# Optimization experiments

Hardware: AMD Instinct MI355X
Metric: run time of the kernel (lower is better)

The kernel has to match this reference:

```python
import jax, jax.numpy as jnp
import numpy as np

N = 50000   # nodes
E = 800000  # edges
D = 128     # input node features
H = 128     # hidden channels
G = 250     # graphs in batch
EPS = 1e-5  # BatchNorm eps


def _lin(k, fi, fo):
    s = 1.0 / np.sqrt(fi)
    return jax.random.uniform(k, (fi, fo), jnp.float32, -s, s)


def setup_inputs() -> dict:
    key = jax.random.key(0)
    ks = jax.random.split(key, 16)
    x = jax.random.normal(ks[0], (N, D), jnp.float32)
    edge_index = jax.random.randint(ks[1], (2, E), 0, N)
    batch = jnp.sort(jax.random.randint(ks[2], (N,), 0, G))
    return {
        "x": x, "edge_index": edge_index, "batch": batch,
        "W1": _lin(ks[3], D, H), "b1": jnp.zeros((H,), jnp.float32),
        "g1": jnp.ones((H,), jnp.float32), "be1": jnp.zeros((H,), jnp.float32),
        "W2": _lin(ks[4], H, H), "b2": jnp.zeros((H,), jnp.float32),
        "g2": jnp.ones((H,), jnp.float32), "be2": jnp.zeros((H,), jnp.float32),
        "W3": _lin(ks[5], H, H), "b3": jnp.zeros((H,), jnp.float32),
        "g3": jnp.ones((H,), jnp.float32), "be3": jnp.zeros((H,), jnp.float32),
        "Wm1": _lin(ks[6], H, H), "bm1": _lin(ks[7], H, 1)[:, 0],
        "Wm2": _lin(ks[8], H, 1), "bm2": _lin(ks[9], 1, 1)[:, 0],
    }


def gcn_conv(x, W, b, src, dst, n):
    # PyG GCNConv: h = x W; add self-loops; symmetric deg^{-1/2} normalization;
    # scatter-add messages from src to dst; add bias.
    h = x @ W                                     # [N, H]
    deg = jnp.zeros((n,), h.dtype).at[dst].add(1.0) + 1.0  # in-degree + self-loop
    dis = deg ** -0.5
    coef = dis[src] * dis[dst]                    # [E]
    agg = jax.ops.segment_sum(h[src] * coef[:, None], dst, num_segments=n)
    return agg + h * (1.0 / deg)[:, None] + b     # self-loop term: norm = 1/deg


def bn_relu(x, g, be):
    # BatchNorm1d training-mode stats (biased variance), then ReLU
    m = jnp.mean(x, axis=0)
    v = jnp.mean((x - m) ** 2, axis=0)
    return jax.nn.relu((x - m) * jax.lax.rsqrt(v + EPS) * g + be)


def reference(x, edge_index, batch, W1, b1, g1, be1, W2, b2, g2, be2,
              W3, b3, g3, be3, Wm1, bm1, Wm2, bm2):
    src, dst = edge_index[0], edge_index[1]
    h = bn_relu(gcn_conv(x, W1, b1, src, dst, N), g1, be1)
    h = bn_relu(gcn_conv(h, W2, b2, src, dst, N), g2, be2)
    h = bn_relu(gcn_conv(h, W3, b3, src, dst, N), g3, be3)
    p = jax.ops.segment_sum(h, batch, num_segments=G)   # global_add_pool -> [G, H]
    p = jax.nn.relu(p @ Wm1 + bm1)                      # dropout is identity (eval)
    return p @ Wm2 + bm2                                # [G, 1]
```

## Files before the change

### kernel.cpp

```cpp
#include <hip/hip_runtime.h>

#define NN 50000
#define NE 800000
#define DD 128
#define NG 250
#define BN_EPS 1e-5f
#define ELLW 64
#define GATHER_BLOCKS 2048
#define NSLOT 128

#define NBK 256
#define BKRANGE 196
#define BKCAP 4608
#define P1_BLOCKS 250
#define P1_CHUNK 3200

typedef unsigned short u16;
typedef __attribute__((ext_vector_type(8))) short bf16x8;
typedef __attribute__((ext_vector_type(4))) float f32x4;

__device__ inline u16 f2bf(float f) {
    union { float f; unsigned u; } c;
    c.f = f;
    unsigned r = c.u + 0x7fffu + ((c.u >> 16) & 1u);
    return (u16)(r >> 16);
}
__device__ inline float bf2f(u16 h) {
    union { unsigned u; float f; } c;
    c.u = (unsigned)h << 16;
    return c.f;
}
__device__ inline unsigned pack2bf(float lo, float hi) {
    return (unsigned)f2bf(lo) | ((unsigned)f2bf(hi) << 16);
}
__device__ inline float bf_lo(unsigned u) {
    union { unsigned u; float f; } c;
    c.u = u << 16;
    return c.f;
}
__device__ inline float bf_hi(unsigned u) {
    union { unsigned u; float f; } c;
    c.u = u & 0xffff0000u;
    return c.f;
}


__global__ __launch_bounds__(256) void binpass_k(const int* __restrict__ src,
                                                 const int* __restrict__ dst,
                                                 int* __restrict__ bcnt,
                                                 unsigned* __restrict__ buckets) {
    __shared__ unsigned bins[NBK][64];
    __shared__ int bn[NBK];
    __shared__ int bbase[NBK];
    int tid = threadIdx.x;
    for (int i = tid; i < NBK; i += 256) bn[i] = 0;
    __syncthreads();
    int e0 = blockIdx.x * P1_CHUNK;
    for (int i = tid; i < P1_CHUNK; i += 256) {
        int e = e0 + i;
        if (e < NE) {
            int d = dst[e];
            int s = src[e];
            int bk = d / BKRANGE;
            int dl = d - bk * BKRANGE;
            unsigned ent = ((unsigned)dl << 16) | (unsigned)s;
            int pos = atomicAdd(&bn[bk], 1);
            if (pos < 64) {
                bins[bk][pos] = ent;
            } else {
                int gb = atomicAdd(&bcnt[bk], 1);
                if (gb < BKCAP) buckets[(size_t)bk * BKCAP + gb] = ent;
            }
        }
    }
    __syncthreads();
    if (tid < NBK) {
        int cnt = bn[tid]; if (cnt > 64) cnt = 64;
        bbase[tid] = cnt ? atomicAdd(&bcnt[tid], cnt) : 0;
    }
    __syncthreads();
    if (tid < NBK) {
        int cnt = bn[tid]; if (cnt > 64) cnt = 64;
        int base = bbase[tid];
        unsigned* gb = buckets + (size_t)tid * BKCAP;
        for (int i = 0; i < cnt; i++) {
            int g = base + i;
            if (g < BKCAP) gb[g] = bins[tid][i];
        }
    }
}


__global__ __launch_bounds__(256) void ellpass_k(const int* __restrict__ bcnt,
                                                 const unsigned* __restrict__ buckets,
                                                 int* __restrict__ fc,
                                                 float* __restrict__ dis,
                                                 u16* __restrict__ ell) {
    __shared__ u16 lell[BKRANGE * ELLW];
    __shared__ int lcnt[BKRANGE];
    int b = blockIdx.x, tid = threadIdx.x;
    for (int i = tid; i < BKRANGE; i += 256) lcnt[i] = 0;
    __syncthreads();
    int cnt = bcnt[b]; if (cnt > BKCAP) cnt = BKCAP;
    const unsigned* bk = buckets + (size_t)b * BKCAP;
    for (int i = tid; i < cnt; i += 256) {
        unsigned ent = bk[i];
        int dl = ent >> 16;
        int pos = atomicAdd(&lcnt[dl], 1);
        if (pos < ELLW) lell[dl * ELLW + pos] = (u16)(ent & 0xffffu);
    }
    __syncthreads();
    int n0 = b * BKRANGE;
    int nrows = NN - n0; if (nrows > BKRANGE) nrows = BKRANGE; if (nrows < 0) nrows = 0;
    int words = nrows * (ELLW / 2);
    unsigned* gell = (unsigned*)(ell + (size_t)n0 * ELLW);
    const unsigned* l32 = (const unsigned*)lell;
    for (int i = tid; i < words; i += 256) gell[i] = l32[i];
    for (int i = tid; i < nrows; i += 256) {
        int c = lcnt[i]; if (c > ELLW) c = ELLW;
        fc[n0 + i] = c;
        dis[n0 + i] = 1.0f / sqrtf((float)(c + 1));
    }
}


__global__ void wprep_k(const float* __restrict__ W1, const float* __restrict__ W2,
                        const float* __restrict__ W3, u16* __restrict__ wt) {
    int lid = blockIdx.x >> 6;
    int idx = (blockIdx.x & 63) * 256 + threadIdx.x;
    const float* W = lid == 0 ? W1 : (lid == 1 ? W2 : W3);
    int k = idx >> 7, n = idx & 127;
    float w = W[idx];
    u16 hi = f2bf(w);
    u16 lo = f2bf(w - bf2f(hi));
    wt[((size_t)lid * 2 + 0) * 16384 + (size_t)n * 128 + k] = hi;
    wt[((size_t)lid * 2 + 1) * 16384 + (size_t)n * 128 + k] = lo;
}


__global__ __launch_bounds__(256) void mgemm_k(const float* __restrict__ A32,
                                               const u16* __restrict__ A16,
                                               const u16* __restrict__ WT,
                                               const float* __restrict__ sc,
                                               const float* __restrict__ sh,
                                               const float* __restrict__ dis,
                                               u16* __restrict__ HB, int use_bn) {
    __shared__ u16 WL[2 * 128 * 128];
    __shared__ float scs[128], shs[128];
    int tid = threadIdx.x;
    if (use_bn && tid < 128) { scs[tid] = sc[tid]; shs[tid] = sh[tid]; }
    {
        const uint4* wg = (const uint4*)WT;
#pragma unroll
        for (int i = 0; i < 16; i++) {
            int ci = tid + i * 256;
            unsigned byte = (unsigned)ci * 16;
            unsigned n = (byte >> 8) & 127;
            unsigned swz = byte ^ ((n & 7) << 4);
            *(uint4*)((char*)WL + swz) = wg[ci];
        }
    }
    __syncthreads();

    int w = tid >> 6, lane = tid & 63;
    int col = lane & 15, lg = lane >> 4;
    int rowA = blockIdx.x * 64 + w * 16 + col;

    union { uint4 q; bf16x8 v; } afr[4];
#pragma unroll
    for (int s = 0; s < 4; s++) afr[s].q = make_uint4(0, 0, 0, 0);
    if (rowA < NN) {
        if (!use_bn) {
            const float4* ap = (const float4*)(A32 + (size_t)rowA * DD);
#pragma unroll
            for (int s = 0; s < 4; s++) {
                float4 f0 = ap[s * 8 + lg * 2];
                float4 f1 = ap[s * 8 + lg * 2 + 1];
                afr[s].q = make_uint4(pack2bf(f0.x, f0.y), pack2bf(f0.z, f0.w),
                                      pack2bf(f1.x, f1.y), pack2bf(f1.z, f1.w));
            }
        } else {
            const uint4* ap = (const uint4*)(A16 + (size_t)rowA * DD);
#pragma unroll
            for (int s = 0; s < 4; s++) {
                uint4 q = ap[s * 4 + lg];
                unsigned uu[4] = {q.x, q.y, q.z, q.w};
                int cbase = s * 32 + lg * 8;
#pragma unroll
                for (int t = 0; t < 4; t++) {
                    int c0 = cbase + t * 2;
                    float f0 = fmaxf(fmaf(bf_lo(uu[t]), scs[c0], shs[c0]), 0.f);
                    float f1 = fmaxf(fmaf(bf_hi(uu[t]), scs[c0 + 1], shs[c0 + 1]), 0.f);
                    uu[t] = pack2bf(f0, f1);
                }
                afr[s].q = make_uint4(uu[0], uu[1], uu[2], uu[3]);
            }
        }
    }

    f32x4 acc[8];
#pragma unroll
    for (int cf = 0; cf < 8; cf++) { acc[cf][0] = 0.f; acc[cf][1] = 0.f; acc[cf][2] = 0.f; acc[cf][3] = 0.f; }

#pragma unroll
    for (int half = 0; half < 2; half++) {
#pragma unroll
        for (int s = 0; s < 4; s++) {
#pragma unroll
            for (int cf = 0; cf < 8; cf++) {
                int nn = cf * 16 + col;
                unsigned byte = (unsigned)half * 32768 + (unsigned)nn * 256
                              + (unsigned)(s * 64 + lg * 16);
                byte ^= ((nn & 7) << 4);
                bf16x8 b = *(const bf16x8*)((const char*)WL + byte);
                acc[cf] = __builtin_amdgcn_mfma_f32_16x16x32_bf16(afr[s].v, b, acc[cf], 0, 0, 0);
            }
        }
    }

#pragma unroll
    for (int r = 0; r < 4; r++) {
        int ro = blockIdx.x * 64 + w * 16 + lg * 4 + r;
        if (ro < NN) {
            float dv = dis[ro];
#pragma unroll
            for (int cf = 0; cf < 8; cf++) {
                HB[(size_t)ro * DD + cf * 16 + col] = f2bf(acc[cf][r] * dv);
            }
        }
    }
}


__global__ __launch_bounds__(256) void gather_k(const u16* __restrict__ HB,
                                                const float* __restrict__ dis,
                                                const int* __restrict__ fc,
                                                const u16* __restrict__ ell,
                                                const float* __restrict__ bias,
                                                u16* __restrict__ AGG,
                                                float* __restrict__ statsP) {
    __shared__ float s_sum[128], s_sq[128];
    int tid = threadIdx.x;
    if (tid < 128) { s_sum[tid] = 0.f; s_sq[tid] = 0.f; }
    __syncthreads();
    int lane = tid & 63;
    int wid = blockIdx.x * 4 + (tid >> 6);
    const int nwaves = GATHER_BLOCKS * 4;
    int c = lane * 2;
    float b0 = bias[c], b1 = bias[c + 1];
    float lsum0 = 0.f, lsum1 = 0.f, lsq0 = 0.f, lsq1 = 0.f;
    for (int v = wid; v < NN; v += nwaves) {
        int cntv = fc[v];
        if (cntv > ELLW) cntv = ELLW;
        int myidx = (lane < cntv) ? (int)ell[(size_t)v * ELLW + lane] : 0;
        float a0 = 0.f, a1 = 0.f;
        int j = 0;
        for (; j + 8 <= cntv; j += 8) {
            unsigned r[8];
#pragma unroll
            for (int q = 0; q < 8; q++) {
                int s = __shfl(myidx, j + q);
                r[q] = *(const unsigned*)(HB + (size_t)s * DD + c);
            }
#pragma unroll
            for (int q = 0; q < 8; q++) { a0 += bf_lo(r[q]); a1 += bf_hi(r[q]); }
        }
        for (; j < cntv; j++) {
            int s = __shfl(myidx, j);
            unsigned r0 = *(const unsigned*)(HB + (size_t)s * DD + c);
            a0 += bf_lo(r0);
            a1 += bf_hi(r0);
        }
        unsigned rsf = *(const unsigned*)(HB + (size_t)v * DD + c);
        float dv = dis[v];
        float o0 = fmaf(a0 + bf_lo(rsf), dv, b0);
        float o1 = fmaf(a1 + bf_hi(rsf), dv, b1);
        *(unsigned*)(AGG + (size_t)v * DD + c) = pack2bf(o0, o1);
        lsum0 += o0; lsum1 += o1;
        lsq0 += o0 * o0; lsq1 += o1 * o1;
    }
    atomicAdd(&s_sum[c], lsum0);
    atomicAdd(&s_sum[c + 1], lsum1);
    atomicAdd(&s_sq[c], lsq0);
    atomicAdd(&s_sq[c + 1], lsq1);
    __syncthreads();
    if (tid < 128) {
        float* slot = statsP + (size_t)(blockIdx.x & (NSLOT - 1)) * 256;
        atomicAdd(&slot[tid], s_sum[tid]);
        atomicAdd(&slot[128 + tid], s_sq[tid]);
    }
}


__global__ void bnfix_k(const float* __restrict__ statsP, const float* __restrict__ g,
                        const float* __restrict__ be, float* __restrict__ sc,
                        float* __restrict__ sh) {
    int c = threadIdx.x;
    float sum = 0.f, sq = 0.f;
    for (int s = 0; s < NSLOT; s++) {
        sum += statsP[(size_t)s * 256 + c];
        sq  += statsP[(size_t)s * 256 + 128 + c];
    }
    float mean = sum * (1.0f / NN);
    float var = sq * (1.0f / NN) - mean * mean;
    float scl = g[c] / sqrtf(var + BN_EPS);
    sc[c] = scl;
    sh[c] = be[c] - mean * scl;
}


__global__ __launch_bounds__(256) void pool_k(const u16* __restrict__ AGG,
                                              const int* __restrict__ batch,
                                              const float* __restrict__ sc,
                                              const float* __restrict__ sh,
                                              float* __restrict__ P) {
    int lane = threadIdx.x & 63;
    int wid = blockIdx.x * 4 + (threadIdx.x >> 6);
    int nw = gridDim.x * 4;
    int c = lane * 2;
    float sc0 = sc[c], sc1 = sc[c + 1], sh0 = sh[c], sh1 = sh[c + 1];
    int chunk = (NN + nw - 1) / nw;
    int v0 = wid * chunk, v1 = v0 + chunk;
    if (v1 > NN) v1 = NN;
    if (v0 >= NN) return;
    int curb = batch[v0];
    float acc0 = 0.f, acc1 = 0.f;
    for (int v = v0; v < v1; v++) {
        int b = batch[v];
        if (b != curb) {
            atomicAdd(&P[curb * 128 + c], acc0);
            atomicAdd(&P[curb * 128 + c + 1], acc1);
            acc0 = 0.f; acc1 = 0.f; curb = b;
        }
        unsigned hv = *(const unsigned*)(AGG + (size_t)v * DD + c);
        acc0 += fmaxf(fmaf(bf_lo(hv), sc0, sh0), 0.f);
        acc1 += fmaxf(fmaf(bf_hi(hv), sc1, sh1), 0.f);
    }
    atomicAdd(&P[curb * 128 + c], acc0);
    atomicAdd(&P[curb * 128 + c + 1], acc1);
}


__global__ __launch_bounds__(128) void head_k(const float* __restrict__ P,
                                              const float* __restrict__ Wm1,
                                              const float* __restrict__ bm1,
                                              const float* __restrict__ Wm2,
                                              const float* __restrict__ bm2,
                                              float* __restrict__ OUT) {
    __shared__ float prow[128];
    __shared__ float red[128];
    int g = blockIdx.x, t = threadIdx.x;
    prow[t] = P[g * 128 + t];
    __syncthreads();
    float acc = bm1[t];
#pragma unroll 8
    for (int i = 0; i < 128; i++) acc = fmaf(prow[i], Wm1[i * 128 + t], acc);
    red[t] = fmaxf(acc, 0.f) * Wm2[t];
    __syncthreads();
    for (int off = 64; off > 0; off >>= 1) {
        if (t < off) red[t] += red[t + off];
        __syncthreads();
    }
    if (t == 0) OUT[g] = red[0] + bm2[0];
}


extern "C" void kernel_launch(void* const* d_in, const int* in_sizes, int n_in,
                              void* d_out, int out_size, void* d_ws, size_t ws_size,
                              hipStream_t stream) {
    const float* x   = (const float*)d_in[0];
    const int*  ei   = (const int*)d_in[1];
    const int*  batch= (const int*)d_in[2];
    const float* W1  = (const float*)d_in[3];
    const float* b1  = (const float*)d_in[4];
    const float* g1  = (const float*)d_in[5];
    const float* be1 = (const float*)d_in[6];
    const float* W2  = (const float*)d_in[7];
    const float* b2  = (const float*)d_in[8];
    const float* g2  = (const float*)d_in[9];
    const float* be2 = (const float*)d_in[10];
    const float* W3  = (const float*)d_in[11];
    const float* b3  = (const float*)d_in[12];
    const float* g3  = (const float*)d_in[13];
    const float* be3 = (const float*)d_in[14];
    const float* Wm1 = (const float*)d_in[15];
    const float* bm1 = (const float*)d_in[16];
    const float* Wm2 = (const float*)d_in[17];
    const float* bm2 = (const float*)d_in[18];
    float* out = (float*)d_out;

    char* ws = (char*)d_ws;
    size_t off = 0;
    auto alloc = [&](size_t bytes) -> void* {
        void* p = ws + off;
        off = (off + bytes + 255) & ~(size_t)255;
        return p;
    };
    int*   fc    = (int*)alloc((size_t)NN * 4);
    float* dis   = (float*)alloc((size_t)NN * 4);
    u16*   ell   = (u16*)alloc((size_t)NN * ELLW * 2);
    u16*   hb    = (u16*)alloc((size_t)NN * DD * 2);
    u16*   agg   = (u16*)alloc((size_t)NN * DD * 2);
    u16*   wt    = (u16*)alloc((size_t)3 * 2 * 16384 * 2);
    float* scb   = (float*)alloc(3 * 128 * 4);
    float* shb   = (float*)alloc(3 * 128 * 4);
    unsigned* buckets = (unsigned*)alloc((size_t)NBK * BKCAP * 4);
    float* statsP= (float*)alloc((size_t)3 * NSLOT * 256 * 4);
    float* p     = (float*)alloc((size_t)NG * DD * 4);
    int*   bcnt  = (int*)alloc((size_t)NBK * 4);

    const int* srcI = ei;
    const int* dstI = ei + NE;

    hipMemsetAsync(statsP, 0, (size_t)3 * NSLOT * 256 * 4 + (size_t)NG * DD * 4 + (size_t)NBK * 4, stream);

    binpass_k<<<P1_BLOCKS, 256, 0, stream>>>(srcI, dstI, bcnt, buckets);
    ellpass_k<<<NBK, 256, 0, stream>>>(bcnt, buckets, fc, dis, ell);
    wprep_k<<<192, 256, 0, stream>>>(W1, W2, W3, wt);

    const int GB = (NN + 63) / 64;
    const size_t SL = (size_t)NSLOT * 256;

    mgemm_k<<<GB, 256, 0, stream>>>(x, nullptr, wt, nullptr, nullptr, dis, hb, 0);
    gather_k<<<GATHER_BLOCKS, 256, 0, stream>>>(hb, dis, fc, ell, b1, agg, statsP);
    bnfix_k<<<1, 128, 0, stream>>>(statsP, g1, be1, scb, shb);

    mgemm_k<<<GB, 256, 0, stream>>>(nullptr, agg, wt + 2 * 16384, scb, shb, dis, hb, 1);
    gather_k<<<GATHER_BLOCKS, 256, 0, stream>>>(hb, dis, fc, ell, b2, agg, statsP + SL);
    bnfix_k<<<1, 128, 0, stream>>>(statsP + SL, g2, be2, scb + 128, shb + 128);

    mgemm_k<<<GB, 256, 0, stream>>>(nullptr, agg, wt + 4 * 16384, scb + 128, shb + 128, dis, hb, 1);
    gather_k<<<GATHER_BLOCKS, 256, 0, stream>>>(hb, dis, fc, ell, b3, agg, statsP + 2 * SL);
    bnfix_k<<<1, 128, 0, stream>>>(statsP + 2 * SL, g3, be3, scb + 256, shb + 256);

    pool_k<<<512, 256, 0, stream>>>(agg, batch, scb + 256, shb + 256, p);
    head_k<<<NG, 128, 0, stream>>>(p, Wm1, bm1, Wm2, bm2, out);
}
```

Baseline: 333.5 us.

## Fold BN stat finalization into consumers and pad ELL rows with zero sentinel

Removes the three single-block bnfix kernels by recomputing BN scale/shift inside each consuming mgemm and pool block, and cuts the stats slot count so that recomputation stays cheap. ELL rows are pre-filled with a sentinel index pointing at an extra zeroed row of hb, and counts are rounded up to a multiple of eight, so the gather loop drops its scalar tail and the lane-bounds check. This saves kernel launches and branchy tail work, at the cost of redundant stat reductions per block, more atomic contention on fewer slots, and some wasted loads of the zero row.

```diff
diff --git a/kernel.cpp b/kernel.cpp
--- a/kernel.cpp
+++ b/kernel.cpp
@@ -7,7 +7,7 @@
 #define BN_EPS 1e-5f
 #define ELLW 64
 #define GATHER_BLOCKS 2048
-#define NSLOT 128
+#define NSLOT 32
 
 #define NBK 256
 #define BKRANGE 196
@@ -95,11 +95,17 @@
                                                  const unsigned* __restrict__ buckets,
                                                  int* __restrict__ fc,
                                                  float* __restrict__ dis,
-                                                 u16* __restrict__ ell) {
+                                                 u16* __restrict__ ell,
+                                                 u16* __restrict__ hb) {
     __shared__ u16 lell[BKRANGE * ELLW];
     __shared__ int lcnt[BKRANGE];
     int b = blockIdx.x, tid = threadIdx.x;
     for (int i = tid; i < BKRANGE; i += 256) lcnt[i] = 0;
+    {
+        unsigned sent2 = ((unsigned)NN << 16) | (unsigned)NN;
+        unsigned* l32 = (unsigned*)lell;
+        for (int i = tid; i < BKRANGE * ELLW / 2; i += 256) l32[i] = sent2;
+    }
     __syncthreads();
     int cnt = bcnt[b]; if (cnt > BKCAP) cnt = BKCAP;
     const unsigned* bk = buckets + (size_t)b * BKCAP;
@@ -118,9 +124,10 @@
     for (int i = tid; i < words; i += 256) gell[i] = l32[i];
     for (int i = tid; i < nrows; i += 256) {
         int c = lcnt[i]; if (c > ELLW) c = ELLW;
-        fc[n0 + i] = c;
+        fc[n0 + i] = (c + 7) & ~7;
         dis[n0 + i] = 1.0f / sqrtf((float)(c + 1));
     }
+    if (b == 0 && tid < 64) ((unsigned*)(hb + (size_t)NN * DD))[tid] = 0;
 }
 
 
@@ -141,14 +148,27 @@
 __global__ __launch_bounds__(256) void mgemm_k(const float* __restrict__ A32,
                                                const u16* __restrict__ A16,
                                                const u16* __restrict__ WT,
-                                               const float* __restrict__ sc,
-                                               const float* __restrict__ sh,
+                                               const float* __restrict__ statsP,
+                                               const float* __restrict__ g,
+                                               const float* __restrict__ be,
                                                const float* __restrict__ dis,
                                                u16* __restrict__ HB, int use_bn) {
     __shared__ u16 WL[2 * 128 * 128];
     __shared__ float scs[128], shs[128];
     int tid = threadIdx.x;
-    if (use_bn && tid < 128) { scs[tid] = sc[tid]; shs[tid] = sh[tid]; }
+    if (use_bn && tid < 128) {
+        float sum = 0.f, sq = 0.f;
+#pragma unroll
+        for (int s = 0; s < NSLOT; s++) {
+            sum += statsP[(size_t)s * 256 + tid];
+            sq  += statsP[(size_t)s * 256 + 128 + tid];
+        }
+        float mean = sum * (1.0f / NN);
+        float var = sq * (1.0f / NN) - mean * mean;
+        float scl = g[tid] / sqrtf(var + BN_EPS);
+        scs[tid] = scl;
+        shs[tid] = be[tid] - mean * scl;
+    }
     {
         const uint4* wg = (const uint4*)WT;
 #pragma unroll
@@ -250,12 +270,10 @@
     float b0 = bias[c], b1 = bias[c + 1];
     float lsum0 = 0.f, lsum1 = 0.f, lsq0 = 0.f, lsq1 = 0.f;
     for (int v = wid; v < NN; v += nwaves) {
-        int cntv = fc[v];
-        if (cntv > ELLW) cntv = ELLW;
-        int myidx = (lane < cntv) ? (int)ell[(size_t)v * ELLW + lane] : 0;
+        int cnt8 = fc[v];
+        int myidx = (int)ell[(size_t)v * ELLW + lane];
         float a0 = 0.f, a1 = 0.f;
-        int j = 0;
-        for (; j + 8 <= cntv; j += 8) {
+        for (int j = 0; j < cnt8; j += 8) {
             unsigned r[8];
 #pragma unroll
             for (int q = 0; q < 8; q++) {
@@ -264,12 +282,6 @@
             }
 #pragma unroll
             for (int q = 0; q < 8; q++) { a0 += bf_lo(r[q]); a1 += bf_hi(r[q]); }
-        }
-        for (; j < cntv; j++) {
-            int s = __shfl(myidx, j);
-            unsigned r0 = *(const unsigned*)(HB + (size_t)s * DD + c);
-            a0 += bf_lo(r0);
-            a1 += bf_hi(r0);
         }
         unsigned rsf = *(const unsigned*)(HB + (size_t)v * DD + c);
         float dv = dis[v];
@@ -292,33 +304,33 @@
 }
 
 
-__global__ void bnfix_k(const float* __restrict__ statsP, const float* __restrict__ g,
-                        const float* __restrict__ be, float* __restrict__ sc,
-                        float* __restrict__ sh) {
-    int c = threadIdx.x;
-    float sum = 0.f, sq = 0.f;
-    for (int s = 0; s < NSLOT; s++) {
-        sum += statsP[(size_t)s * 256 + c];
-        sq  += statsP[(size_t)s * 256 + 128 + c];
-    }
-    float mean = sum * (1.0f / NN);
-    float var = sq * (1.0f / NN) - mean * mean;
-    float scl = g[c] / sqrtf(var + BN_EPS);
-    sc[c] = scl;
-    sh[c] = be[c] - mean * scl;
-}
-
-
 __global__ __launch_bounds__(256) void pool_k(const u16* __restrict__ AGG,
                                               const int* __restrict__ batch,
-                                              const float* __restrict__ sc,
-                                              const float* __restrict__ sh,
+                                              const float* __restrict__ statsP,
+                                              const float* __restrict__ g,
+                                              const float* __restrict__ be,
                                               float* __restrict__ P) {
-    int lane = threadIdx.x & 63;
-    int wid = blockIdx.x * 4 + (threadIdx.x >> 6);
+    __shared__ float psc[128], psh[128];
+    int tid = threadIdx.x;
+    if (tid < 128) {
+        float sum = 0.f, sq = 0.f;
+#pragma unroll
+        for (int s = 0; s < NSLOT; s++) {
+            sum += statsP[(size_t)s * 256 + tid];
+            sq  += statsP[(size_t)s * 256 + 128 + tid];
+        }
+        float mean = sum * (1.0f / NN);
+        float var = sq * (1.0f / NN) - mean * mean;
+        float scl = g[tid] / sqrtf(var + BN_EPS);
+        psc[tid] = scl;
+        psh[tid] = be[tid] - mean * scl;
+    }
+    __syncthreads();
+    int lane = tid & 63;
+    int wid = blockIdx.x * 4 + (tid >> 6);
     int nw = gridDim.x * 4;
     int c = lane * 2;
-    float sc0 = sc[c], sc1 = sc[c + 1], sh0 = sh[c], sh1 = sh[c + 1];
+    float sc0 = psc[c], sc1 = psc[c + 1], sh0 = psh[c], sh1 = psh[c + 1];
     int chunk = (NN + nw - 1) / nw;
     int v0 = wid * chunk, v1 = v0 + chunk;
     if (v1 > NN) v1 = NN;
@@ -399,11 +411,9 @@
     int*   fc    = (int*)alloc((size_t)NN * 4);
     float* dis   = (float*)alloc((size_t)NN * 4);
     u16*   ell   = (u16*)alloc((size_t)NN * ELLW * 2);
-    u16*   hb    = (u16*)alloc((size_t)NN * DD * 2);
+    u16*   hb    = (u16*)alloc((size_t)(NN + 1) * DD * 2);
     u16*   agg   = (u16*)alloc((size_t)NN * DD * 2);
     u16*   wt    = (u16*)alloc((size_t)3 * 2 * 16384 * 2);
-    float* scb   = (float*)alloc(3 * 128 * 4);
-    float* shb   = (float*)alloc(3 * 128 * 4);
     unsigned* buckets = (unsigned*)alloc((size_t)NBK * BKCAP * 4);
     float* statsP= (float*)alloc((size_t)3 * NSLOT * 256 * 4);
     float* p     = (float*)alloc((size_t)NG * DD * 4);
@@ -415,24 +425,21 @@
     hipMemsetAsync(statsP, 0, (size_t)3 * NSLOT * 256 * 4 + (size_t)NG * DD * 4 + (size_t)NBK * 4, stream);
 
     binpass_k<<<P1_BLOCKS, 256, 0, stream>>>(srcI, dstI, bcnt, buckets);
-    ellpass_k<<<NBK, 256, 0, stream>>>(bcnt, buckets, fc, dis, ell);
+    ellpass_k<<<NBK, 256, 0, stream>>>(bcnt, buckets, fc, dis, ell, hb);
     wprep_k<<<192, 256, 0, stream>>>(W1, W2, W3, wt);
 
     const int GB = (NN + 63) / 64;
     const size_t SL = (size_t)NSLOT * 256;
 
-    mgemm_k<<<GB, 256, 0, stream>>>(x, nullptr, wt, nullptr, nullptr, dis, hb, 0);
+    mgemm_k<<<GB, 256, 0, stream>>>(x, nullptr, wt, nullptr, nullptr, nullptr, dis, hb, 0);
     gather_k<<<GATHER_BLOCKS, 256, 0, stream>>>(hb, dis, fc, ell, b1, agg, statsP);
-    bnfix_k<<<1, 128, 0, stream>>>(statsP, g1, be1, scb, shb);
-
-    mgemm_k<<<GB, 256, 0, stream>>>(nullptr, agg, wt + 2 * 16384, scb, shb, dis, hb, 1);
+
+    mgemm_k<<<GB, 256, 0, stream>>>(nullptr, agg, wt + 2 * 16384, statsP, g1, be1, dis, hb, 1);
     gather_k<<<GATHER_BLOCKS, 256, 0, stream>>>(hb, dis, fc, ell, b2, agg, statsP + SL);
-    bnfix_k<<<1, 128, 0, stream>>>(statsP + SL, g2, be2, scb + 128, shb + 128);
-
-    mgemm_k<<<GB, 256, 0, stream>>>(nullptr, agg, wt + 4 * 16384, scb + 128, shb + 128, dis, hb, 1);
+
+    mgemm_k<<<GB, 256, 0, stream>>>(nullptr, agg, wt + 4 * 16384, statsP + SL, g2, be2, dis, hb, 1);
     gather_k<<<GATHER_BLOCKS, 256, 0, stream>>>(hb, dis, fc, ell, b3, agg, statsP + 2 * SL);
-    bnfix_k<<<1, 128, 0, stream>>>(statsP + 2 * SL, g3, be3, scb + 256, shb + 256);
-
-    pool_k<<<512, 256, 0, stream>>>(agg, batch, scb + 256, shb + 256, p);
+
+    pool_k<<<512, 256, 0, stream>>>(agg, batch, statsP + 2 * SL, g3, be3, p);
     head_k<<<NG, 128, 0, stream>>>(p, Wm1, bm1, Wm2, bm2, out);
 }
```

New measurement: 313.4 us. 1.06x faster.
